# Performance work log

Measured on AMD Instinct MI355X. Metric: run time of the kernel, lower is better.

## Reference

```python
import jax, jax.numpy as jnp
import numpy as np

B, T, L = 8, 5, 16          # meta-batch, inner (train) steps, test examples per task
C, H, W = 3, 64, 64
NCLS = 100
FEAT = 256 * (H // 16) * (W // 16)  # 4096
CHANS = [(C, 32), (32, 64), (64, 128), (128, 256), (256, 256)]
DN = ('NCHW', 'OIHW', 'NCHW')


def setup_inputs() -> dict:
    key = jax.random.key(0)
    ks = jax.random.split(key, 16)
    inp = {}
    for j, (ic, oc) in enumerate(CHANS):
        std = 1.0 / np.sqrt(ic * 9)
        inp[f"w{j}"] = jax.random.normal(ks[j], (oc, ic, 3, 3), jnp.float32) * std
        inp[f"b{j}"] = jnp.zeros((oc,), jnp.float32)
    inp["W_out"] = jax.random.normal(ks[5], (NCLS, FEAT), jnp.float32) / np.sqrt(FEAT)
    inp["b_out"] = jnp.zeros((NCLS,), jnp.float32)
    inp["inner_log_lr"] = jnp.asarray(np.log(0.01), jnp.float32)
    inp["train_x"] = jax.random.normal(ks[6], (B, T, C, H, W), jnp.float32)
    inp["test_x"] = jax.random.normal(ks[7], (B, L, C, H, W), jnp.float32)
    inp["train_gate"] = jax.random.uniform(ks[8], (B, T, FEAT), dtype=jnp.float32)
    inp["test_gate"] = jax.random.uniform(ks[9], (B, L, FEAT), dtype=jnp.float32)
    inp["train_y"] = jax.random.randint(ks[10], (B, T), 0, NCLS)
    inp["test_y"] = jax.random.randint(ks[11], (B, L), 0, NCLS)
    inp["evaluate"] = 1
    return inp


def _conv(x, w, b, s):
    # x: [N, C, H, W]; per-example weight w: [OC, IC, 3, 3]; 'same'-ish pad=1
    y = jax.lax.conv_general_dilated(x, w, (s, s), [(1, 1), (1, 1)], dimension_numbers=DN)
    return jax.nn.relu(y + b[None, :, None, None])


def _features(fw, x, gate):
    # x: [B, L, C, H, W]; fw: tuple of per-example (batched) params
    for j in range(5):
        s = 1 if j == 0 else 2
        x = jax.vmap(_conv, in_axes=(0, 0, 0, None))(x, fw[2 * j], fw[2 * j + 1], s)
    return x.reshape(x.shape[0], x.shape[1], -1) * gate  # [B, L, FEAT]


def _ce(logits, y):
    return -jnp.take_along_axis(jax.nn.log_softmax(logits, -1), y[..., None], -1)[..., 0]


def _forward(params, log_lr, train_x, test_x, train_gate, test_gate, train_y, test_y):
    b = train_x.shape[0]
    lr = jnp.exp(log_lr)
    # per-example fast weights (MAML)
    fw = tuple(jnp.broadcast_to(p, (b,) + p.shape) for p in params)

    def step(fw, batch):
        xi, yi, gi = batch  # [B,C,H,W], [B], [B,FEAT]
        def loss_fn(fw):
            f = _features(fw, xi[:, None], gi[:, None])[:, 0]  # [B, FEAT]
            logit = jnp.einsum('bnm,bm->bn', fw[10], f) + fw[11]
            return _ce(logit, yi).sum()
        g = jax.grad(loss_fn)(fw)
        return tuple(w - lr * gw for w, gw in zip(fw, g)), None

    fw, _ = jax.lax.scan(
        step, fw,
        (jnp.swapaxes(train_x, 0, 1), jnp.swapaxes(train_y, 0, 1), jnp.swapaxes(train_gate, 0, 1)))

    f = _features(fw, test_x, test_gate)                         # [B, L, FEAT]
    logit = jnp.einsum('bnm,blm->bln', fw[10], f) + fw[11][:, None, :]
    loss = _ce(logit, test_y)[..., None]                          # [B, L, 1]
    return loss, lr, logit


def reference(w0, b0, w1, b1, w2, b2, w3, b3, w4, b4, W_out, b_out, inner_log_lr,
              train_x, test_x, train_gate, test_gate, train_y, test_y, evaluate):
    params = (w0, b0, w1, b1, w2, b2, w3, b3, w4, b4, W_out, b_out)
    loss, lr, logit = _forward(params, inner_log_lr, train_x, test_x,
                               train_gate, test_gate, train_y, test_y)
    evaluation = (jnp.argmax(logit, -1) == test_y) if evaluate else None
    return (loss, lr, evaluation, logit)
```

## Files before the change

kernel.cpp:

```cpp
#include <hip/hip_runtime.h>

#define NB 8
#define NT 5
#define NL 16
#define NCLS 100
#define FEAT 4096
#define CHW (3*64*64)

#define OFF_W0 0
#define OFF_B0 864
#define OFF_W1 896
#define OFF_B1 19328
#define OFF_W2 19392
#define OFF_B2 93120
#define OFF_W3 93248
#define OFF_B3 388160
#define OFF_W4 388416
#define OFF_B4 978240
#define OFF_WO 978496
#define OFF_BO 1388096
#define PT     1388196

#define A1 0
#define A2 131072
#define A3 196608
#define A4 229376
#define A5 245760
#define ATOT 249856

struct Params12 { const float* p[12]; };

__global__ void bcast_kernel(Params12 ps, float* __restrict__ fw) {
    const int offs[13] = {OFF_W0,OFF_B0,OFF_W1,OFF_B1,OFF_W2,OFF_B2,OFF_W3,OFF_B3,
                          OFF_W4,OFF_B4,OFF_WO,OFF_BO,PT};
    long idx = (long)blockIdx.x * blockDim.x + threadIdx.x;
    long total = (long)NB * PT;
    if (idx >= total) return;
    int i = (int)(idx % PT);
    int j = 11;
    while (j > 0 && i < offs[j]) --j;
    fw[idx] = ps.p[j][i - offs[j]];
}

template<int IC,int IH,int IW,int OC,int OH,int OW,int S,int UF,int BS>
__global__ __launch_bounds__(BS) void conv_fwd_u(
    const float* __restrict__ xb, long x_ts,
    const float* __restrict__ fw, int woff, int boff,
    float* __restrict__ yb, long y_ts)
{
    constexpr int OHW = OH*OW, IHW = IH*IW;
    long idx = (long)blockIdx.x * BS + threadIdx.x;
    int pix = (int)(idx % OHW); long r = idx / OHW;
    int oc = (int)(r % OC); int b = (int)(r / OC);
    int oh = pix / OW, ow = pix % OW;
    int ih0 = oh*S - 1, iw0 = ow*S - 1;

    const float* x = xb + (long)b * x_ts;
    const float* w = fw + (long)b * PT + woff + (long)oc * IC * 9;
    float acc = fw[(long)b * PT + boff + oc];

    #pragma unroll 1
    for (int ic0 = 0; ic0 < IC; ic0 += UF) {
        float xv[UF][9];
        #pragma unroll
        for (int u = 0; u < UF; ++u) {
            const float* xc = x + (long)(ic0 + u) * IHW;
            #pragma unroll
            for (int kh = 0; kh < 3; ++kh) {
                int ih = ih0 + kh;
                #pragma unroll
                for (int kw = 0; kw < 3; ++kw) {
                    int iw = iw0 + kw;
                    bool v = ((unsigned)ih < (unsigned)IH) && ((unsigned)iw < (unsigned)IW);
                    xv[u][kh*3+kw] = v ? xc[ih*IW + iw] : 0.f;
                }
            }
        }
        #pragma unroll
        for (int u = 0; u < UF; ++u) {
            const float* wc = w + (ic0 + u) * 9;
            #pragma unroll
            for (int k = 0; k < 9; ++k)
                acc += xv[u][k] * wc[k];
        }
    }
    yb[(long)b * y_ts + (long)oc * OHW + pix] = fmaxf(acc, 0.f);
}

template<int IC,int IH,int IW,int OC,int OH,int OW,int S,int UF,int BS,int KS>
__global__ __launch_bounds__(BS) void conv_fwd_uks(
    const float* __restrict__ xb, long x_ts,
    const float* __restrict__ fw, int woff,
    float* __restrict__ pb)
{
    constexpr int OHW = OH*OW, IHW = IH*IW;
    constexpr int ICC = IC/KS;
    long idx = (long)blockIdx.x * BS + threadIdx.x;
    int pix = (int)(idx % OHW); long r = idx / OHW;
    int oc = (int)(r % OC); r /= OC;
    int ks = (int)(r % KS); int b = (int)(r / KS);
    int oh = pix / OW, ow = pix % OW;
    int ih0 = oh*S - 1, iw0 = ow*S - 1;

    const float* x = xb + (long)b * x_ts;
    const float* w = fw + (long)b * PT + woff + (long)oc * IC * 9;
    float acc = 0.f;

    #pragma unroll 1
    for (int ic0 = ks*ICC; ic0 < (ks+1)*ICC; ic0 += UF) {
        float xv[UF][9];
        #pragma unroll
        for (int u = 0; u < UF; ++u) {
            const float* xc = x + (long)(ic0 + u) * IHW;
            #pragma unroll
            for (int kh = 0; kh < 3; ++kh) {
                int ih = ih0 + kh;
                #pragma unroll
                for (int kw = 0; kw < 3; ++kw) {
                    int iw = iw0 + kw;
                    bool v = ((unsigned)ih < (unsigned)IH) && ((unsigned)iw < (unsigned)IW);
                    xv[u][kh*3+kw] = v ? xc[ih*IW + iw] : 0.f;
                }
            }
        }
        #pragma unroll
        for (int u = 0; u < UF; ++u) {
            const float* wc = w + (ic0 + u) * 9;
            #pragma unroll
            for (int k = 0; k < 9; ++k)
                acc += xv[u][k] * wc[k];
        }
    }
    pb[((long)ks*NB + b) * ((long)OC*OHW) + (long)oc*OHW + pix] = acc;
}

template<int IC,int IH,int IW,int OC,int OH,int OW,int S,int UF,int KS>
__global__ __launch_bounds__(64) void conv_fwd_us(
    const float* __restrict__ xb, long x_ts,
    const float* __restrict__ fw, int woff,
    float* __restrict__ pb)
{
    constexpr int OHW = OH*OW, IHW = IH*IW, ICC = IC/KS;
    static_assert(OHW == 64, "one wave = one oc-plane");
    int bi = blockIdx.x;
    int oc = bi % OC; int ks = (bi / OC) % KS; int b = bi / (OC*KS);
    int pix = threadIdx.x;
    int oh = pix / OW, ow = pix % OW;
    int ih0 = oh*S - 1, iw0 = ow*S - 1;

    const float* x = xb + (long)b * x_ts;
    const float* w = fw + (long)b * PT + woff + (long)oc * IC * 9;

    float acc = 0.f;
    #pragma unroll 1
    for (int ic0 = ks*ICC; ic0 < (ks+1)*ICC; ic0 += UF) {
        float xv[UF][9];
        #pragma unroll
        for (int u = 0; u < UF; ++u) {
            const float* xc = x + (long)(ic0 + u) * IHW;
            #pragma unroll
            for (int kh = 0; kh < 3; ++kh) {
                int ih = ih0 + kh;
                #pragma unroll
                for (int kw = 0; kw < 3; ++kw) {
                    int iw = iw0 + kw;
                    bool v = ((unsigned)ih < (unsigned)IH) && ((unsigned)iw < (unsigned)IW);
                    xv[u][kh*3+kw] = v ? xc[ih*IW + iw] : 0.f;
                }
            }
        }
        #pragma unroll
        for (int u = 0; u < UF; ++u) {
            const float* wc = w + (ic0 + u) * 9;
            #pragma unroll
            for (int k = 0; k < 9; ++k)
                acc += xv[u][k] * wc[k];
        }
    }
    pb[((long)ks*NB + b) * ((long)OC*OHW) + (long)oc*OHW + pix] = acc;
}

template<int IC,int IH,int IW,int OC,int OH,int OW,int S,int TOC,int NSUB,int ICB>
__global__ __launch_bounds__(256) void conv_fwd2(
    const float* __restrict__ xb, long x_ts, long x_es,
    const float* __restrict__ fw, int woff, int boff,
    float* __restrict__ yb, long y_ts, int N)
{
    constexpr int OHW = OH*OW, IHW = IH*IW;
    constexpr int PPB = 256/NSUB;
    constexpr int TILES = OHW/PPB;
    constexpr int OCB = NSUB*TOC;
    constexpr int NOCG = OC/OCB;
    __shared__ float wlds[ICB*9*OCB];

    int bi = blockIdx.x;
    int tile = bi % TILES;
    int ocg  = (bi / TILES) % NOCG;
    int n    = (bi / (TILES*NOCG)) % N;
    int b    = bi / (TILES*NOCG*N);

    int tid = threadIdx.x;
    int pixl = tid % PPB, sub = tid / PPB;
    int pix = tile * PPB + pixl;
    int oc0 = ocg * OCB + sub * TOC;
    int oh = pix / OW, ow = pix % OW;
    int ih0 = oh*S - 1, iw0 = ow*S - 1;

    const float* xp  = xb + (long)b * x_ts + (long)n * x_es;
    const float* fwp = fw + (long)b * PT + woff;
    const float* bp  = fw + (long)b * PT + boff;

    float acc[TOC];
    #pragma unroll
    for (int t = 0; t < TOC; ++t) acc[t] = bp[oc0 + t];

    #pragma unroll 1
    for (int ic0i = 0; ic0i < IC; ic0i += ICB) {
        __syncthreads();
        for (int i = tid; i < ICB*9*OCB; i += 256) {
            int o = i % OCB; int rem = i / OCB; int k = rem % 9; int icb = rem / 9;
            wlds[i] = fwp[((long)(ocg*OCB + o) * IC + ic0i + icb) * 9 + k];
        }
        __syncthreads();
        #pragma unroll 2
        for (int icb = 0; icb < ICB; ++icb) {
            const float* xc = xp + (long)(ic0i + icb) * IHW;
            float xv[9];
            #pragma unroll
            for (int kh = 0; kh < 3; ++kh)
            #pragma unroll
            for (int kw = 0; kw < 3; ++kw) {
                int ih = ih0 + kh, iw = iw0 + kw;
                bool v = ((unsigned)ih < (unsigned)IH) && ((unsigned)iw < (unsigned)IW);
                xv[kh*3+kw] = v ? xc[ih*IW + iw] : 0.f;
            }
            const float* wl = wlds + icb*9*OCB + sub*TOC;
            #pragma unroll
            for (int k = 0; k < 9; ++k) {
                #pragma unroll
                for (int t = 0; t < TOC; ++t)
                    acc[t] += xv[k] * wl[k*OCB + t];
            }
        }
    }

    float* yp = yb + (long)b * y_ts;
    #pragma unroll
    for (int t = 0; t < TOC; ++t)
        yp[((long)n*OC + oc0 + t) * OHW + pix] = fmaxf(acc[t], 0.f);
}

template<int IC,int IH,int IW,int OC,int OH,int OW,int S,
         int NG,int TH,int ICB,int KS,int NTOT>
__global__ __launch_bounds__(256) void conv_fwd_gx(
    const float* __restrict__ xb, long x_ts, long x_es,
    const float* __restrict__ fw, int woff, int boff,
    float* __restrict__ yb, long y_ts,
    float* __restrict__ pb)
{
    constexpr int OHW = OH*OW, IHW = IH*IW;
    constexpr int TOC = 16, OCB2 = 4*TOC;
    constexpr int NOCG = OC/OCB2;
    constexpr int RT = OH/TH;
    constexpr int NGRP = NTOT/NG;
    constexpr int ICC = IC/KS;
    constexpr int PW = IW + 1;
    constexpr int PROWS = (TH-1)*S + 3;
    constexpr int XPR = PROWS*PW;
    constexpr int XP = XPR | 1;
    static_assert(NG*TH*OW == 64, "lanes must cover exactly 64 pixels");
    static_assert(S == 2, "padding derivation assumes stride 2");
    static_assert(ICC % ICB == 0, "chunking");

    __shared__ float xs[NG*ICB*XP];

    int bi = blockIdx.x;
    int ocg = bi % NOCG;
    int rt  = (bi / NOCG) % RT;
    int ng  = (bi / (NOCG*RT)) % NGRP;
    int ks  = (bi / (NOCG*RT*NGRP)) % KS;
    int b   = bi / (NOCG*RT*NGRP*KS);

    int tid = threadIdx.x;
    int pl = tid & 63;
    int ocsub = __builtin_amdgcn_readfirstlane(tid >> 6);
    int nl = pl / (TH*OW);
    int prow = (pl / OW) % TH;
    int pcol = pl % OW;
    int oc0 = ocg*OCB2 + ocsub*TOC;

    const float* xbb = xb + (long)b * x_ts + (long)(ng*NG) * x_es;
    const float* wb  = fw + (long)b * PT + woff;

    float acc[TOC];
    #pragma unroll
    for (int t = 0; t < TOC; ++t)
        acc[t] = (KS == 1) ? fw[(long)b*PT + boff + oc0 + t] : 0.f;

    const int ih0t = rt*TH*S - 1;

    #pragma unroll 1
    for (int c = 0; c < ICC/ICB; ++c) {
        int ic0 = ks*ICC + c*ICB;
        if (c) __syncthreads();
        for (int i = tid; i < NG*ICB*XPR; i += 256) {
            int cc = i % PW;
            int r  = (i / PW) % PROWS;
            int icb = (i / (PW*PROWS)) % ICB;
            int nl2 = i / (PW*PROWS*ICB);
            int ih = ih0t + r, iw = cc - 1;
            float v = 0.f;
            if (ih >= 0 && iw >= 0)
                v = xbb[(long)nl2 * x_es + (long)(ic0+icb)*IHW + ih*IW + iw];
            xs[(nl2*ICB + icb)*XP + r*PW + cc] = v;
        }
        __syncthreads();
        #pragma unroll 2
        for (int icb = 0; icb < ICB; ++icb) {
            int ic = ic0 + icb;
            const float* xr = xs + (nl*ICB + icb)*XP + (prow*S)*PW + pcol*S;
            float xv[9];
            #pragma unroll
            for (int kh = 0; kh < 3; ++kh)
                #pragma unroll
                for (int kw = 0; kw < 3; ++kw)
                    xv[kh*3+kw] = xr[kh*PW + kw];
            const float* wr = wb + ((long)oc0*IC + ic)*9;
            #pragma unroll
            for (int t = 0; t < TOC; ++t) {
                const float* wt = wr + (long)t*IC*9;
                #pragma unroll
                for (int k = 0; k < 9; ++k)
                    acc[t] += xv[k] * wt[k];
            }
        }
    }

    int n = ng*NG + nl;
    int pix = (rt*TH + prow)*OW + pcol;
    if (KS == 1) {
        float* yp = yb + (long)b * y_ts;
        #pragma unroll
        for (int t = 0; t < TOC; ++t)
            yp[((long)n*OC + oc0 + t)*OHW + pix] = fmaxf(acc[t], 0.f);
    } else {
        float* yp = pb + ((long)ks*NB + b) * ((long)NTOT*OC*OHW);
        #pragma unroll
        for (int t = 0; t < TOC; ++t)
            yp[((long)n*OC + oc0 + t)*OHW + pix] = acc[t];
    }
}

template<int KS>
__global__ __launch_bounds__(256) void ksum_relu(
    const float* __restrict__ pb, const float* __restrict__ fw, int boff,
    float* __restrict__ yb, long y_ts, int N, int OC, int OHW)
{
    long plane = (long)N * OC * OHW;
    long idx = (long)blockIdx.x * 256 + threadIdx.x;
    long total = (long)NB * plane;
    if (idx >= total) return;
    int b = (int)(idx / plane);
    long rem = idx % plane;
    int oc = (int)((rem / OHW) % OC);
    float s = fw[(long)b * PT + boff + oc];
    #pragma unroll
    for (int ks = 0; ks < KS; ++ks)
        s += pb[((long)ks * NB + b) * plane + rem];
    yb[(long)b * y_ts + rem] = fmaxf(s, 0.f);
}

template<int IC,int IH,int IW,int OC,int OH,int OW,int S,int OCT,int ICT,int OCPT,int OHC>
__global__ __launch_bounds__(256) void conv_bwd_dwg(
    float* __restrict__ fw, int woff, int boff,
    const float* __restrict__ dzbuf, int dz_off,
    const float* __restrict__ xb, long x_ts,
    const float* __restrict__ loglr)
{
    constexpr int OHW = OH*OW, IHW = IH*IW;
    constexpr int IW2 = IW + 2;
    constexpr int RW  = OHC*S + 1;
    constexpr int XPRAW = RW * IW2;
    constexpr int XP = XPRAW | 1;
    constexpr int OHWC = OHC*OW;
    constexpr int DZP = OHWC + 1;
    constexpr int NCH = OH/OHC;
    constexpr int OCSL = OCT/OCPT;
    static_assert(OCSL*ICT == 256, "block must be 256 threads");
    static_assert((OW & (OW-1)) == 0, "OW power of two");
    constexpr int LOG_OW = (OW==4) ? 2 : ((OW==8) ? 3 : 4);
    constexpr int NOCG = OC/OCT, NICG = IC/ICT;

    __shared__ float dzs[OCT*DZP];
    __shared__ float xs[ICT*XP];

    int bi = blockIdx.x;
    int icg = bi % NICG;
    int ocg = (bi / NICG) % NOCG;
    int b   = bi / (NICG*NOCG);
    int oc0 = ocg*OCT, ic0 = icg*ICT;

    int tid = threadIdx.x;
    int ic_sub = tid % ICT;
    int oc_sub = tid / ICT;

    const float* dzp = dzbuf + (long)b*ATOT + dz_off + (long)oc0*OHW;
    const float* xp  = xb + (long)b*x_ts + (long)ic0*IHW;

    float acc[OCPT][9];
    float accb[OCPT];
    #pragma unroll
    for (int p = 0; p < OCPT; ++p) {
        accb[p] = 0.f;
        #pragma unroll
        for (int k = 0; k < 9; ++k) acc[p][k] = 0.f;
    }

    for (int c = 0; c < NCH; ++c) {
        if (c) __syncthreads();
        for (int i = tid; i < OCT*OHWC; i += 256) {
            int oc = i / OHWC, j = i % OHWC;
            dzs[oc*DZP + j] = dzp[(long)oc*OHW + c*OHWC + j];
        }
        for (int i = tid; i < ICT*XPRAW; i += 256) {
            int ic = i / XPRAW, j = i % XPRAW;
            int r = j / IW2, col = j % IW2;
            int ih = c*(OHC*S) - 1 + r;
            int iw = col - 1;
            float v = 0.f;
            if ((unsigned)ih < (unsigned)IH && (unsigned)iw < (unsigned)IW)
                v = xp[(long)ic*IHW + ih*IW + iw];
            xs[ic*XP + j] = v;
        }
        __syncthreads();

        const float* dzr = dzs + oc_sub*DZP;
        const float* xr0 = xs + ic_sub*XP;
        #pragma unroll 2
        for (int pos = 0; pos < OHWC; ++pos) {
            int ohl = pos >> LOG_OW;
            int ow  = pos & (OW-1);
            const float* xr = xr0 + (ohl*S)*IW2 + ow*S;
            float xv[9];
            #pragma unroll
            for (int kh = 0; kh < 3; ++kh)
                #pragma unroll
                for (int kw = 0; kw < 3; ++kw)
                    xv[kh*3+kw] = xr[kh*IW2 + kw];
            #pragma unroll
            for (int p = 0; p < OCPT; ++p) {
                float dzv = dzr[p*OCSL*DZP + pos];
                accb[p] += dzv;
                #pragma unroll
                for (int k = 0; k < 9; ++k) acc[p][k] += dzv * xv[k];
            }
        }
    }

    float lr = expf(loglr[0]);
    #pragma unroll
    for (int p = 0; p < OCPT; ++p) {
        int oc = oc0 + p*OCSL + oc_sub;
        float* wp = fw + (long)b*PT + woff + ((long)oc*IC + ic0 + ic_sub)*9;
        #pragma unroll
        for (int k = 0; k < 9; ++k) wp[k] -= lr * acc[p][k];
        if (ic_sub == 0 && icg == 0)
            fw[(long)b*PT + boff + oc] -= lr * accb[p];
    }
}

__global__ void head_fwd(const float* __restrict__ a5b, long a_ts, long a_es,
                         const float* __restrict__ gb, long g_ts, long g_es,
                         const float* __restrict__ fw,
                         float* __restrict__ ob, long o_ts, long o_es, int N)
{
    int wid = (int)(((long)blockIdx.x * blockDim.x + threadIdx.x) >> 6);
    int lane = threadIdx.x & 63;
    int total = NB * N * NCLS;
    if (wid >= total) return;
    int cls = wid % NCLS; int r = wid / NCLS;
    int n = r % N; int b = r / N;
    const float* a5 = a5b + (long)b * a_ts + (long)n * a_es;
    const float* g  = gb  + (long)b * g_ts + (long)n * g_es;
    const float* W  = fw + (long)b * PT + OFF_WO + (long)cls * FEAT;
    float acc = 0.f;
    for (int m = lane; m < FEAT; m += 64) acc += W[m] * a5[m] * g[m];
    for (int off = 32; off; off >>= 1) acc += __shfl_down(acc, off, 64);
    if (lane == 0)
        ob[(long)b * o_ts + (long)n * o_es + cls] = acc + fw[(long)b * PT + OFF_BO + cls];
}

__global__ void softmax_dlogit(const float* __restrict__ logi, const int* __restrict__ ty, int t,
                               float* __restrict__ dlog)
{
    __shared__ float red[128];
    int b = blockIdx.x, tid = threadIdx.x;
    const float* lo = logi + b * NCLS;
    float v = (tid < NCLS) ? lo[tid] : -1e30f;
    red[tid] = v; __syncthreads();
    for (int s2 = 64; s2; s2 >>= 1) { if (tid < s2) red[tid] = fmaxf(red[tid], red[tid + s2]); __syncthreads(); }
    float mx = red[0]; __syncthreads();
    float e = (tid < NCLS) ? expf(v - mx) : 0.f;
    red[tid] = e; __syncthreads();
    for (int s2 = 64; s2; s2 >>= 1) { if (tid < s2) red[tid] += red[tid + s2]; __syncthreads(); }
    float sum = red[0];
    if (tid < NCLS) {
        int y = ty[b * NT + t];
        dlog[b * NCLS + tid] = e / sum - (tid == y ? 1.f : 0.f);
    }
}

__global__ void head_bwd_dz5(const float* __restrict__ fw, const float* __restrict__ dlog,
                             const float* __restrict__ ain, const float* __restrict__ gb, long g_ts,
                             float* __restrict__ dz)
{
    int idx = blockIdx.x * blockDim.x + threadIdx.x;
    if (idx >= NB * FEAT) return;
    int m = idx % FEAT, b = idx / FEAT;
    const float* W = fw + (long)b * PT + OFF_WO;
    float df = 0.f;
    for (int c = 0; c < NCLS; ++c) df += W[(long)c * FEAT + m] * dlog[b * NCLS + c];
    float a = ain[(long)b * ATOT + A5 + m];
    dz[(long)b * ATOT + A5 + m] = (a > 0.f) ? df * gb[(long)b * g_ts + m] : 0.f;
}

__global__ void head_update(float* __restrict__ fw, const float* __restrict__ dlog,
                            const float* __restrict__ ain, const float* __restrict__ gb, long g_ts,
                            const float* __restrict__ loglr)
{
    long idx = (long)blockIdx.x * blockDim.x + threadIdx.x;
    long total = (long)NB * NCLS * FEAT;
    if (idx >= total) return;
    int m = (int)(idx % FEAT); long r = idx / FEAT;
    int c = (int)(r % NCLS); int b = (int)(r / NCLS);
    float lr = expf(loglr[0]);
    float f = ain[(long)b * ATOT + A5 + m] * gb[(long)b * g_ts + m];
    float dl = dlog[b * NCLS + c];
    fw[(long)b * PT + OFF_WO + (long)c * FEAT + m] -= lr * dl * f;
    if (m == 0) fw[(long)b * PT + OFF_BO + c] -= lr * dl;
}

template<int IC,int IH,int IW,int OC,int OH,int OW,int ICG,int BLK>
__global__ __launch_bounds__(BLK) void conv_bwd_dx2(
    const float* __restrict__ dzbuf, int dz_off,
    const float* __restrict__ fw, int woff,
    const float* __restrict__ ain, int ain_off,
    float* __restrict__ dzin, int dzin_off)
{
    constexpr int IHW = IH*IW, OHW = OH*OW, NICG = IC/ICG, PB = IHW/BLK;
    __shared__ float wlds[OC*9*ICG];
    int bi = blockIdx.x;
    int pb  = bi % PB;
    int icg = (bi / PB) % NICG;
    int b   = bi / (PB * NICG);
    int ic0 = icg * ICG;
    const float* fwp = fw + (long)b * PT + woff;
    for (int i = threadIdx.x; i < OC*9*ICG; i += BLK) {
        int g = i % ICG; int rem = i / ICG; int k = rem % 9; int oc = rem / 9;
        wlds[i] = fwp[((long)oc * IC + ic0 + g) * 9 + k];
    }
    __syncthreads();

    int pix = pb * BLK + threadIdx.x;
    int ih = pix / IW, iw = pix % IW;
    int kh0 = (ih + 1) & 1, kw0 = (iw + 1) & 1;
    int ohA = (ih + 1 - kh0) >> 1, owA = (iw + 1 - kw0) >> 1;
    float mhA = (ohA < OH) ? 1.f : 0.f;   float mhB = (kh0 == 0) ? 1.f : 0.f;
    float mwA = (owA < OW) ? 1.f : 0.f;   float mwB = (kw0 == 0) ? 1.f : 0.f;
    int ohB = ohA - 1, owB = owA - 1;
    int ohAc = (ohA < OH) ? ohA : 0;  int owAc = (owA < OW) ? owA : 0;
    int ohBc = (ohB >= 0) ? ohB : 0;  int owBc = (owB >= 0) ? owB : 0;

    int oAA = ohAc*OW + owAc; float mAA = mhA*mwA; int kAA = kh0*3 + kw0;
    int oAB = ohAc*OW + owBc; float mAB = mhA*mwB; int kAB = kh0*3 + kw0 + 2;
    int oBA = ohBc*OW + owAc; float mBA = mhB*mwA; int kBA = (kh0+2)*3 + kw0;
    int oBB = ohBc*OW + owBc; float mBB = mhB*mwB; int kBB = (kh0+2)*3 + kw0 + 2;

    const float* dzp = dzbuf + (long)b * ATOT + dz_off;
    float acc[ICG];
    #pragma unroll
    for (int g = 0; g < ICG; ++g) acc[g] = 0.f;

    for (int oc = 0; oc < OC; ++oc) {
        const float* dzo = dzp + oc * OHW;
        float dAA = dzo[oAA] * mAA;
        float dAB = dzo[oAB] * mAB;
        float dBA = dzo[oBA] * mBA;
        float dBB = dzo[oBB] * mBB;
        const float* w = wlds + oc * 9 * ICG;
        #pragma unroll
        for (int g = 0; g < ICG; ++g)
            acc[g] += dAA * w[kAA*ICG+g] + dAB * w[kAB*ICG+g]
                    + dBA * w[kBA*ICG+g] + dBB * w[kBB*ICG+g];
    }
    #pragma unroll
    for (int g = 0; g < ICG; ++g) {
        long p = (long)b * ATOT + (long)(ic0 + g) * IHW + pix;
        float a = ain[p + ain_off];
        dzin[p + dzin_off] = (a > 0.f) ? acc[g] : 0.f;
    }
}

template<int IC,int IH,int IW,int OC,int OH,int OW,int S>
__global__ __launch_bounds__(64) void conv_bwd_dw2(
    float* __restrict__ fw, int woff, int boff,
    const float* __restrict__ dzbuf, int dz_off,
    const float* __restrict__ xb, long x_ts,
    const float* __restrict__ loglr)
{
    constexpr int OHW = OH*OW;
    int bi = blockIdx.x;
    int ic = bi % IC; int oc = (bi / IC) % OC; int b = bi / (IC * OC);
    int lane = threadIdx.x;
    const float* dzp = dzbuf + (long)b * ATOT + dz_off + (long)oc * OHW;
    const float* xp  = xb + (long)b * x_ts + (long)ic * IH * IW;

    float acc[10];
    #pragma unroll
    for (int k = 0; k < 10; ++k) acc[k] = 0.f;

    for (int pos = lane; pos < OHW; pos += 64) {
        float dzv = dzp[pos];
        int oh = pos / OW, ow = pos % OW;
        int ihb = oh * S - 1, iwb = ow * S - 1;
        acc[9] += dzv;
        #pragma unroll
        for (int kh = 0; kh < 3; ++kh) {
            int ih = ihb + kh;
            bool hv = ((unsigned)ih < (unsigned)IH);
            #pragma unroll
            for (int kw = 0; kw < 3; ++kw) {
                int iw = iwb + kw;
                float xv = (hv && (unsigned)iw < (unsigned)IW) ? xp[ih * IW + iw] : 0.f;
                acc[kh*3+kw] += dzv * xv;
            }
        }
    }
    #pragma unroll
    for (int k = 0; k < 10; ++k)
        for (int off = 32; off; off >>= 1) acc[k] += __shfl_down(acc[k], off, 64);

    if (lane == 0) {
        float lr = expf(loglr[0]);
        float* wp = fw + (long)b * PT + woff + ((long)oc * IC + ic) * 9;
        #pragma unroll
        for (int k = 0; k < 9; ++k) wp[k] -= lr * acc[k];
        if (ic == 0) fw[(long)b * PT + boff + oc] -= lr * acc[9];
    }
}

template<int IC,int IH,int IW,int OC,int OH,int OW,int S,int NSP>
__global__ __launch_bounds__(64) void conv_bwd_dw2s(
    float* __restrict__ pbuf,
    const float* __restrict__ dzbuf, int dz_off,
    const float* __restrict__ xb, long x_ts)
{
    constexpr int OHW = OH*OW, CH = OHW/NSP;
    int bi = blockIdx.x;
    int sp = bi % NSP; int ic = (bi / NSP) % IC;
    int oc = (bi / (NSP*IC)) % OC; int b = bi / (NSP*IC*OC);
    int lane = threadIdx.x;
    const float* dzp = dzbuf + (long)b * ATOT + dz_off + (long)oc * OHW;
    const float* xp  = xb + (long)b * x_ts + (long)ic * IH * IW;

    float acc[10];
    #pragma unroll
    for (int k = 0; k < 10; ++k) acc[k] = 0.f;

    for (int pos = sp*CH + lane; pos < sp*CH + CH; pos += 64) {
        float dzv = dzp[pos];
        int oh = pos / OW, ow = pos % OW;
        int ihb = oh * S - 1, iwb = ow * S - 1;
        acc[9] += dzv;
        #pragma unroll
        for (int kh = 0; kh < 3; ++kh) {
            int ih = ihb + kh;
            bool hv = ((unsigned)ih < (unsigned)IH);
            #pragma unroll
            for (int kw = 0; kw < 3; ++kw) {
                int iw = iwb + kw;
                float xv = (hv && (unsigned)iw < (unsigned)IW) ? xp[ih * IW + iw] : 0.f;
                acc[kh*3+kw] += dzv * xv;
            }
        }
    }
    #pragma unroll
    for (int k = 0; k < 10; ++k)
        for (int off = 32; off; off >>= 1) acc[k] += __shfl_down(acc[k], off, 64);

    if (lane == 0) {
        float* pp = pbuf + ((((long)sp*NB + b)*OC + oc)*IC + ic)*10;
        #pragma unroll
        for (int k = 0; k < 10; ++k) pp[k] = acc[k];
    }
}

template<int NSP>
__global__ void dw_finalize(const float* __restrict__ pbuf, float* __restrict__ fw,
                            int woff, int boff, const float* __restrict__ loglr,
                            int OC, int IC)
{
    int idx = blockIdx.x * blockDim.x + threadIdx.x;
    int total = NB * OC * IC * 10;
    if (idx >= total) return;
    int k = idx % 10; int r = idx / 10;
    int ic = r % IC; r /= IC;
    int oc = r % OC; int b = r / OC;
    float s = 0.f;
    #pragma unroll
    for (int sp = 0; sp < NSP; ++sp)
        s += pbuf[((((long)sp*NB + b)*OC + oc)*IC + ic)*10 + k];
    float lr = expf(loglr[0]);
    if (k < 9)
        fw[(long)b*PT + woff + ((long)oc*IC + ic)*9 + k] -= lr * s;
    else if (ic == 0)
        fw[(long)b*PT + boff + oc] -= lr * s;
}

__global__ void final_loss_eval(const float* __restrict__ logit_base,
                                const int* __restrict__ test_y,
                                float* __restrict__ out, int l0, int Lc)
{
    int idx = blockIdx.x * blockDim.x + threadIdx.x;
    if (idx >= NB * Lc) return;
    int n = idx % Lc, b = idx / Lc;
    int l = l0 + n;
    const float* lo = logit_base + ((long)b * NL + l) * NCLS;
    float mx = -1e30f; int am = 0;
    for (int c = 0; c < NCLS; ++c) { float v = lo[c]; if (v > mx) { mx = v; am = c; } }
    float se = 0.f;
    for (int c = 0; c < NCLS; ++c) se += expf(lo[c] - mx);
    int y = test_y[b * NL + l];
    out[b * NL + l] = -(lo[y] - mx - logf(se));
    out[129 + b * NL + l] = (am == y) ? 1.f : 0.f;
}

__global__ void write_lr(const float* __restrict__ loglr, float* __restrict__ out)
{
    if (threadIdx.x == 0 && blockIdx.x == 0) out[128] = expf(loglr[0]);
}

extern "C" void kernel_launch(void* const* d_in, const int* in_sizes, int n_in,
                              void* d_out, int out_size, void* d_ws, size_t ws_size,
                              hipStream_t stream)
{
    const float* loglr      = (const float*)d_in[12];
    const float* train_x    = (const float*)d_in[13];
    const float* test_x     = (const float*)d_in[14];
    const float* train_gate = (const float*)d_in[15];
    const float* test_gate  = (const float*)d_in[16];
    const int*   train_y    = (const int*)d_in[17];
    const int*   test_y     = (const int*)d_in[18];
    float* out = (float*)d_out;

    const long base = (long)NB*PT + 2L*NB*ATOT + 2L*NB*NCLS;
    int LCr = 4;
    if (ws_size >= (size_t)(base + 16L*1572864) * 4) LCr = 16;
    else if (ws_size >= (size_t)(base + 8L*1572864) * 4) LCr = 8;

    float* ws   = (float*)d_ws;
    float* FWp  = ws;
    float* AINp = FWp  + (long)NB * PT;
    float* DZp  = AINp + (long)NB * ATOT;
    float* LOGIp= DZp  + (long)NB * ATOT;
    float* DLOGp= LOGIp + NB * NCLS;
    float* TAp  = DLOGp + NB * NCLS;
    float* TBp  = TAp + (long)NB * LCr * 131072;

    float* P3t = TAp;
    float* P4t = TAp + 262144;
    float* PW0 = TAp + 262144 + 131072;

    Params12 ps;
    for (int j = 0; j < 12; ++j) ps.p[j] = (const float*)d_in[j];
    {
        long tot = (long)NB * PT;
        bcast_kernel<<<(int)((tot + 255) / 256), 256, 0, stream>>>(ps, FWp);
    }

    for (int t = 0; t < NT; ++t) {
        conv_fwd_u<3,64,64,32,64,64,1,3,256><<<4096, 256, 0, stream>>>(
            train_x + (long)t * CHW, (long)NT * CHW, FWp, OFF_W0, OFF_B0, AINp + A1, (long)ATOT);
        conv_fwd_u<32,64,64,64,32,32,2,4,256><<<2048, 256, 0, stream>>>(
            AINp + A1, (long)ATOT, FWp, OFF_W1, OFF_B1, AINp + A2, (long)ATOT);
        conv_fwd_u<64,32,32,128,16,16,2,4,256><<<1024, 256, 0, stream>>>(
            AINp + A2, (long)ATOT, FWp, OFF_W2, OFF_B2, AINp + A3, (long)ATOT);
        conv_fwd_us<128,16,16,256,8,8,2,4, 2><<<NB*2*256, 64, 0, stream>>>(
            AINp + A3, (long)ATOT, FWp, OFF_W3, P3t);
        ksum_relu<2><<<(NB*256*64 + 255) / 256, 256, 0, stream>>>(
            P3t, FWp, OFF_B3, AINp + A4, (long)ATOT, 1, 256, 64);
        conv_fwd_uks<256,8,8,256,4,4,2,8,64, 4><<<2048, 64, 0, stream>>>(
            AINp + A4, (long)ATOT, FWp, OFF_W4, P4t);
        ksum_relu<4><<<(NB*256*16 + 255) / 256, 256, 0, stream>>>(
            P4t, FWp, OFF_B4, AINp + A5, (long)ATOT, 1, 256, 16);

        {
            long waves = (long)NB * NCLS;
            head_fwd<<<(int)((waves * 64 + 255) / 256), 256, 0, stream>>>(
                AINp + A5, (long)ATOT, 0,
                train_gate + (long)t * FEAT, (long)NT * FEAT, 0,
                FWp, LOGIp, (long)NCLS, 0, 1);
        }
        softmax_dlogit<<<NB, 128, 0, stream>>>(LOGIp, train_y, t, DLOGp);
        head_bwd_dz5<<<(NB * FEAT + 255) / 256, 256, 0, stream>>>(
            FWp, DLOGp, AINp, train_gate + (long)t * FEAT, (long)NT * FEAT, DZp);
        {
            long tot = (long)NB * NCLS * FEAT;
            head_update<<<(int)((tot + 255) / 256), 256, 0, stream>>>(
                FWp, DLOGp, AINp, train_gate + (long)t * FEAT, (long)NT * FEAT, loglr);
        }

        conv_bwd_dx2<256,8,8,256,4,4,2,64><<<8*128, 64, 0, stream>>>(
            DZp, A5, FWp, OFF_W4, AINp, A4, DZp, A4);
        conv_bwd_dwg<256,8,8,256,4,4,2, 64,8,2, 4><<<1024, 256, 0, stream>>>(
            FWp, OFF_W4, OFF_B4, DZp, A5, AINp + A4, (long)ATOT, loglr);

        conv_bwd_dx2<128,16,16,256,8,8,4,256><<<8*32, 256, 0, stream>>>(
            DZp, A4, FWp, OFF_W3, AINp, A3, DZp, A3);
        conv_bwd_dwg<128,16,16,256,8,8,2, 64,8,2, 8><<<512, 256, 0, stream>>>(
            FWp, OFF_W3, OFF_B3, DZp, A4, AINp + A3, (long)ATOT, loglr);

        conv_bwd_dx2<64,32,32,128,16,16,4,256><<<8*16*4, 256, 0, stream>>>(
            DZp, A3, FWp, OFF_W2, AINp, A2, DZp, A2);
        conv_bwd_dwg<64,32,32,128,16,16,2, 32,8,1, 4><<<256, 256, 0, stream>>>(
            FWp, OFF_W2, OFF_B2, DZp, A3, AINp + A2, (long)ATOT, loglr);

        conv_bwd_dx2<32,64,64,64,32,32,4,256><<<8*8*16, 256, 0, stream>>>(
            DZp, A2, FWp, OFF_W1, AINp, A1, DZp, A1);
        conv_bwd_dw2<32,64,64,64,32,32,2><<<8*64*32, 64, 0, stream>>>(
            FWp, OFF_W1, OFF_B1, DZp, A2, AINp + A1, (long)ATOT, loglr);
        conv_bwd_dw2s<3,64,64,32,64,64,1, 8><<<8*32*3*8, 64, 0, stream>>>(
            PW0, DZp, A1, train_x + (long)t * CHW, (long)NT * CHW);
        dw_finalize<8><<<(NB*32*3*10 + 255) / 256, 256, 0, stream>>>(
            PW0, FWp, OFF_W0, OFF_B0, loglr, 32, 3);
    }

    if (LCr == 16) {
        conv_fwd2<3,64,64,32,64,64,1, 32,1,3><<<NB*16*16, 256, 0, stream>>>(
            test_x, (long)NL * CHW, CHW,
            FWp, OFF_W0, OFF_B0, TAp, 16L * 131072, 16);

        conv_fwd_gx<32,64,64, 64,32,32, 2, 1,2,8, 1, 16><<<2048, 256, 0, stream>>>(
            TAp, 16L*131072, 131072, FWp, OFF_W1, OFF_B1, TBp, 16L*65536, nullptr);
        conv_fwd_gx<64,32,32, 128,16,16, 2, 1,4,8, 1, 16><<<1024, 256, 0, stream>>>(
            TBp, 16L*65536, 65536, FWp, OFF_W2, OFF_B2, TAp, 16L*32768, nullptr);
        {
            float* P3 = TAp + 4194304;
            conv_fwd_gx<128,16,16, 256,8,8, 2, 1,8,8, 4, 16><<<2048, 256, 0, stream>>>(
                TAp, 16L*32768, 32768, FWp, OFF_W3, 0, nullptr, 0, P3);
            ksum_relu<4><<<(int)(((long)NB*16*256*64 + 255) / 256), 256, 0, stream>>>(
                P3, FWp, OFF_B3, TBp, 16L * 16384, 16, 256, 64);
        }
        {
            float* P4 = TBp + 2097152;
            conv_fwd_gx<256,8,8, 256,4,4, 2, 4,4,8, 8, 16><<<1024, 256, 0, stream>>>(
                TBp, 16L*16384, 16384, FWp, OFF_W4, 0, nullptr, 0, P4);
            ksum_relu<8><<<(int)(((long)NB*16*256*16 + 255) / 256), 256, 0, stream>>>(
                P4, FWp, OFF_B4, TAp, 16L * 4096, 16, 256, 16);
        }
        {
            long waves = (long)NB * 16 * NCLS;
            head_fwd<<<(int)((waves * 64 + 255) / 256), 256, 0, stream>>>(
                TAp, 16L * FEAT, FEAT,
                test_gate, (long)NL * FEAT, FEAT,
                FWp, out + 257, (long)NL * NCLS, NCLS, 16);
        }
    } else {
        for (int c = 0; c < NL / LCr; ++c) {
            int l0 = c * LCr;
            conv_fwd2<3,64,64,32,64,64,1, 32,1,3><<<NB*LCr*16, 256, 0, stream>>>(
                test_x + (long)l0 * CHW, (long)NL * CHW, CHW,
                FWp, OFF_W0, OFF_B0, TAp, (long)LCr * 131072, LCr);
            conv_fwd2<32,64,64,64,32,32,2, 16,1,8><<<NB*LCr*16, 256, 0, stream>>>(
                TAp, (long)LCr * 131072, 131072,
                FWp, OFF_W1, OFF_B1, TBp, (long)LCr * 65536, LCr);
            conv_fwd2<64,32,32,128,16,16,2, 16,1,8><<<NB*LCr*8, 256, 0, stream>>>(
                TBp, (long)LCr * 65536, 65536,
                FWp, OFF_W2, OFF_B2, TAp, (long)LCr * 32768, LCr);
            conv_fwd2<128,16,16,256,8,8,2, 8,4,8><<<NB*LCr*8, 256, 0, stream>>>(
                TAp, (long)LCr * 32768, 32768,
                FWp, OFF_W3, OFF_B3, TBp, (long)LCr * 16384, LCr);
            conv_fwd2<256,8,8,256,4,4,2, 4,16,8><<<NB*LCr*4, 256, 0, stream>>>(
                TBp, (long)LCr * 16384, 16384,
                FWp, OFF_W4, OFF_B4, TAp, (long)LCr * 4096, LCr);
            {
                long waves = (long)NB * LCr * NCLS;
                head_fwd<<<(int)((waves * 64 + 255) / 256), 256, 0, stream>>>(
                    TAp, (long)LCr * FEAT, FEAT,
                    test_gate + (long)l0 * FEAT, (long)NL * FEAT, FEAT,
                    FWp, out + 257 + (long)l0 * NCLS, (long)NL * NCLS, NCLS, LCr);
            }
        }
    }
    final_loss_eval<<<(NB * NL + 255) / 256, 256, 0, stream>>>(
        out + 257, test_y, out, 0, NL);
    write_lr<<<1, 1, 0, stream>>>(loglr, out);
}
```

Measured before the change: 4.170 ms.

## Split backward dx convolutions over output channels and halve forward tile widths

Adds a split-K variant of the stride-2 backward input-gradient kernel that partitions output channels across blocks, writes partial sums to a scratch buffer, then reduces them with a ReLU-mask kernel. This raises block count for the small late layers, which had few blocks. Separately, the per-wave output-channel count in the grouped forward conv is now a template parameter, and two test-time layers use 8 instead of 16 with doubled grids. The cost is extra partial-sum memory traffic, an extra launch per layer, and less weight reuse per thread.

```diff
diff --git a/kernel.cpp b/kernel.cpp
--- a/kernel.cpp
+++ b/kernel.cpp
@@ -251,7 +251,7 @@
 }
 
 template<int IC,int IH,int IW,int OC,int OH,int OW,int S,
-         int NG,int TH,int ICB,int KS,int NTOT>
+         int NG,int TH,int ICB,int KS,int NTOT,int TOCP>
 __global__ __launch_bounds__(256) void conv_fwd_gx(
     const float* __restrict__ xb, long x_ts, long x_es,
     const float* __restrict__ fw, int woff, int boff,
@@ -259,7 +259,7 @@
     float* __restrict__ pb)
 {
     constexpr int OHW = OH*OW, IHW = IH*IW;
-    constexpr int TOC = 16, OCB2 = 4*TOC;
+    constexpr int OCB2 = 4*TOCP;
     constexpr int NOCG = OC/OCB2;
     constexpr int RT = OH/TH;
     constexpr int NGRP = NTOT/NG;
@@ -287,14 +287,14 @@
     int nl = pl / (TH*OW);
     int prow = (pl / OW) % TH;
     int pcol = pl % OW;
-    int oc0 = ocg*OCB2 + ocsub*TOC;
+    int oc0 = ocg*OCB2 + ocsub*TOCP;
 
     const float* xbb = xb + (long)b * x_ts + (long)(ng*NG) * x_es;
     const float* wb  = fw + (long)b * PT + woff;
 
-    float acc[TOC];
-    #pragma unroll
-    for (int t = 0; t < TOC; ++t)
+    float acc[TOCP];
+    #pragma unroll
+    for (int t = 0; t < TOCP; ++t)
         acc[t] = (KS == 1) ? fw[(long)b*PT + boff + oc0 + t] : 0.f;
 
     const int ih0t = rt*TH*S - 1;
@@ -327,7 +327,7 @@
                     xv[kh*3+kw] = xr[kh*PW + kw];
             const float* wr = wb + ((long)oc0*IC + ic)*9;
             #pragma unroll
-            for (int t = 0; t < TOC; ++t) {
+            for (int t = 0; t < TOCP; ++t) {
                 const float* wt = wr + (long)t*IC*9;
                 #pragma unroll
                 for (int k = 0; k < 9; ++k)
@@ -341,12 +341,12 @@
     if (KS == 1) {
         float* yp = yb + (long)b * y_ts;
         #pragma unroll
-        for (int t = 0; t < TOC; ++t)
+        for (int t = 0; t < TOCP; ++t)
             yp[((long)n*OC + oc0 + t)*OHW + pix] = fmaxf(acc[t], 0.f);
     } else {
         float* yp = pb + ((long)ks*NB + b) * ((long)NTOT*OC*OHW);
         #pragma unroll
-        for (int t = 0; t < TOC; ++t)
+        for (int t = 0; t < TOCP; ++t)
             yp[((long)n*OC + oc0 + t)*OHW + pix] = acc[t];
     }
 }
@@ -601,6 +601,86 @@
     }
 }
 
+template<int IC,int IH,int IW,int OC,int OH,int OW,int ICG,int BLK,int KOS>
+__global__ __launch_bounds__(BLK) void conv_bwd_dx2k(
+    const float* __restrict__ dzbuf, int dz_off,
+    const float* __restrict__ fw, int woff,
+    float* __restrict__ pbuf)
+{
+    constexpr int IHW = IH*IW, OHW = OH*OW, NICG = IC/ICG, PB = IHW/BLK;
+    constexpr int OCC = OC/KOS;
+    __shared__ float wlds[OCC*9*ICG];
+    int bi = blockIdx.x;
+    int pb  = bi % PB;
+    int icg = (bi / PB) % NICG;
+    int kos = (bi / (PB * NICG)) % KOS;
+    int b   = bi / (PB * NICG * KOS);
+    int ic0 = icg * ICG;
+    int ocb = kos * OCC;
+    const float* fwp = fw + (long)b * PT + woff;
+    for (int i = threadIdx.x; i < OCC*9*ICG; i += BLK) {
+        int g = i % ICG; int rem = i / ICG; int k = rem % 9; int ocl = rem / 9;
+        wlds[i] = fwp[((long)(ocb + ocl) * IC + ic0 + g) * 9 + k];
+    }
+    __syncthreads();
+
+    int pix = pb * BLK + threadIdx.x;
+    int ih = pix / IW, iw = pix % IW;
+    int kh0 = (ih + 1) & 1, kw0 = (iw + 1) & 1;
+    int ohA = (ih + 1 - kh0) >> 1, owA = (iw + 1 - kw0) >> 1;
+    float mhA = (ohA < OH) ? 1.f : 0.f;   float mhB = (kh0 == 0) ? 1.f : 0.f;
+    float mwA = (owA < OW) ? 1.f : 0.f;   float mwB = (kw0 == 0) ? 1.f : 0.f;
+    int ohB = ohA - 1, owB = owA - 1;
+    int ohAc = (ohA < OH) ? ohA : 0;  int owAc = (owA < OW) ? owA : 0;
+    int ohBc = (ohB >= 0) ? ohB : 0;  int owBc = (owB >= 0) ? owB : 0;
+
+    int oAA = ohAc*OW + owAc; float mAA = mhA*mwA; int kAA = kh0*3 + kw0;
+    int oAB = ohAc*OW + owBc; float mAB = mhA*mwB; int kAB = kh0*3 + kw0 + 2;
+    int oBA = ohBc*OW + owAc; float mBA = mhB*mwA; int kBA = (kh0+2)*3 + kw0;
+    int oBB = ohBc*OW + owBc; float mBB = mhB*mwB; int kBB = (kh0+2)*3 + kw0 + 2;
+
+    const float* dzp = dzbuf + (long)b * ATOT + dz_off;
+    float acc[ICG];
+    #pragma unroll
+    for (int g = 0; g < ICG; ++g) acc[g] = 0.f;
+
+    for (int ocl = 0; ocl < OCC; ++ocl) {
+        const float* dzo = dzp + (ocb + ocl) * OHW;
+        float dAA = dzo[oAA] * mAA;
+        float dAB = dzo[oAB] * mAB;
+        float dBA = dzo[oBA] * mBA;
+        float dBB = dzo[oBB] * mBB;
+        const float* w = wlds + ocl * 9 * ICG;
+        #pragma unroll
+        for (int g = 0; g < ICG; ++g)
+            acc[g] += dAA * w[kAA*ICG+g] + dAB * w[kAB*ICG+g]
+                    + dBA * w[kBA*ICG+g] + dBB * w[kBB*ICG+g];
+    }
+    float* pp = pbuf + ((long)kos * NB + b) * ((long)IC * IHW);
+    #pragma unroll
+    for (int g = 0; g < ICG; ++g)
+        pp[(long)(ic0 + g) * IHW + pix] = acc[g];
+}
+
+template<int KOS>
+__global__ __launch_bounds__(256) void ksum_dx(
+    const float* __restrict__ pbuf, const float* __restrict__ ain, int ain_off,
+    float* __restrict__ dzin, int dzin_off, long ichw)
+{
+    long idx = (long)blockIdx.x * 256 + threadIdx.x;
+    long total = (long)NB * ichw;
+    if (idx >= total) return;
+    int b = (int)(idx / ichw);
+    long rem = idx % ichw;
+    float s = 0.f;
+    #pragma unroll
+    for (int kos = 0; kos < KOS; ++kos)
+        s += pbuf[((long)kos * NB + b) * ichw + rem];
+    long p = (long)b * ATOT + rem;
+    float a = ain[p + ain_off];
+    dzin[p + dzin_off] = (a > 0.f) ? s : 0.f;
+}
+
 template<int IC,int IH,int IW,int OC,int OH,int OW,int S>
 __global__ __launch_bounds__(64) void conv_bwd_dw2(
     float* __restrict__ fw, int woff, int boff,
@@ -770,6 +850,7 @@
     float* P3t = TAp;
     float* P4t = TAp + 262144;
     float* PW0 = TAp + 262144 + 131072;
+    float* PDX = TAp + 458752;
 
     Params12 ps;
     for (int j = 0; j < 12; ++j) ps.p[j] = (const float*)d_in[j];
@@ -810,18 +891,24 @@
                 FWp, DLOGp, AINp, train_gate + (long)t * FEAT, (long)NT * FEAT, loglr);
         }
 
-        conv_bwd_dx2<256,8,8,256,4,4,2,64><<<8*128, 64, 0, stream>>>(
-            DZp, A5, FWp, OFF_W4, AINp, A4, DZp, A4);
+        conv_bwd_dx2k<256,8,8,256,4,4,2,64, 4><<<4096, 64, 0, stream>>>(
+            DZp, A5, FWp, OFF_W4, PDX);
+        ksum_dx<4><<<(int)(((long)NB*16384 + 255) / 256), 256, 0, stream>>>(
+            PDX, AINp, A4, DZp, A4, 16384);
         conv_bwd_dwg<256,8,8,256,4,4,2, 64,8,2, 4><<<1024, 256, 0, stream>>>(
             FWp, OFF_W4, OFF_B4, DZp, A5, AINp + A4, (long)ATOT, loglr);
 
-        conv_bwd_dx2<128,16,16,256,8,8,4,256><<<8*32, 256, 0, stream>>>(
-            DZp, A4, FWp, OFF_W3, AINp, A3, DZp, A3);
+        conv_bwd_dx2k<128,16,16,256,8,8,4,256, 4><<<1024, 256, 0, stream>>>(
+            DZp, A4, FWp, OFF_W3, PDX);
+        ksum_dx<4><<<(int)(((long)NB*32768 + 255) / 256), 256, 0, stream>>>(
+            PDX, AINp, A3, DZp, A3, 32768);
         conv_bwd_dwg<128,16,16,256,8,8,2, 64,8,2, 8><<<512, 256, 0, stream>>>(
             FWp, OFF_W3, OFF_B3, DZp, A4, AINp + A3, (long)ATOT, loglr);
 
-        conv_bwd_dx2<64,32,32,128,16,16,4,256><<<8*16*4, 256, 0, stream>>>(
-            DZp, A3, FWp, OFF_W2, AINp, A2, DZp, A2);
+        conv_bwd_dx2k<64,32,32,128,16,16,4,256, 2><<<1024, 256, 0, stream>>>(
+            DZp, A3, FWp, OFF_W2, PDX);
+        ksum_dx<2><<<(int)(((long)NB*65536 + 255) / 256), 256, 0, stream>>>(
+            PDX, AINp, A2, DZp, A2, 65536);
         conv_bwd_dwg<64,32,32,128,16,16,2, 32,8,1, 4><<<256, 256, 0, stream>>>(
             FWp, OFF_W2, OFF_B2, DZp, A3, AINp + A2, (long)ATOT, loglr);
 
@@ -840,20 +927,20 @@
             test_x, (long)NL * CHW, CHW,
             FWp, OFF_W0, OFF_B0, TAp, 16L * 131072, 16);
 
-        conv_fwd_gx<32,64,64, 64,32,32, 2, 1,2,8, 1, 16><<<2048, 256, 0, stream>>>(
+        conv_fwd_gx<32,64,64, 64,32,32, 2, 1,2,8, 1, 16, 16><<<2048, 256, 0, stream>>>(
             TAp, 16L*131072, 131072, FWp, OFF_W1, OFF_B1, TBp, 16L*65536, nullptr);
-        conv_fwd_gx<64,32,32, 128,16,16, 2, 1,4,8, 1, 16><<<1024, 256, 0, stream>>>(
+        conv_fwd_gx<64,32,32, 128,16,16, 2, 1,4,8, 1, 16, 8><<<2048, 256, 0, stream>>>(
             TBp, 16L*65536, 65536, FWp, OFF_W2, OFF_B2, TAp, 16L*32768, nullptr);
         {
             float* P3 = TAp + 4194304;
-            conv_fwd_gx<128,16,16, 256,8,8, 2, 1,8,8, 4, 16><<<2048, 256, 0, stream>>>(
+            conv_fwd_gx<128,16,16, 256,8,8, 2, 1,8,8, 4, 16, 16><<<2048, 256, 0, stream>>>(
                 TAp, 16L*32768, 32768, FWp, OFF_W3, 0, nullptr, 0, P3);
             ksum_relu<4><<<(int)(((long)NB*16*256*64 + 255) / 256), 256, 0, stream>>>(
                 P3, FWp, OFF_B3, TBp, 16L * 16384, 16, 256, 64);
         }
         {
             float* P4 = TBp + 2097152;
-            conv_fwd_gx<256,8,8, 256,4,4, 2, 4,4,8, 8, 16><<<1024, 256, 0, stream>>>(
+            conv_fwd_gx<256,8,8, 256,4,4, 2, 4,4,8, 8, 16, 8><<<2048, 256, 0, stream>>>(
                 TBp, 16L*16384, 16384, FWp, OFF_W4, 0, nullptr, 0, P4);
             ksum_relu<8><<<(int)(((long)NB*16*256*16 + 255) / 256), 256, 0, stream>>>(
                 P4, FWp, OFF_B4, TAp, 16L * 4096, 16, 256, 16);
```

Result: faster. 3.848 ms (-7.7%).
